# Kernel tuning notes

Measured on AMD Instinct MI355X. Metric: run time of the kernel, lower is better.

The kernel has to match this reference:

```python
import jax, jax.numpy as jnp
import numpy as np

K_V_DIM = 100
_SQRT_D = float(np.sqrt(K_V_DIM))


def _dk_layer(q, k, v, Wq, bq, Wk, n_unsqueeze):
    """One DKEncoder_layer: DK_text + DK_knowledge + DK_fusion (CokeBert attention).
    q: [B, q_dim]; k: [..., n, K_V_DIM]; v: [..., n, d_v].
    Attention over the last neighbor axis n.
    """
    # DK_text: linear + tanh + unsqueeze to broadcast against k
    q_i = jnp.tanh(q @ Wq.T + bq)                               # [B, D]
    q_i = q_i.reshape((q_i.shape[0],) + (1,) * n_unsqueeze + (K_V_DIM,))
    # DK_knowledge: bias-free linear on k
    k = k @ Wk.T
    # DK_fusion (CokeBert): scaled dot, mask zeros, leaky_relu+softmax, zero out fully-masked rows
    attn = (q_i * k).sum(-1) / _SQRT_D                          # [..., n]
    attn = jnp.where(attn == 0.0, -10000.0, attn)
    attn = jax.nn.softmax(jax.nn.leaky_relu(attn), axis=-1)
    n = attn.shape[-1]
    attn = jnp.where(attn == 1.0 / n, 0.0, attn)
    return jnp.einsum('...n,...nd->...d', attn, v)              # [..., d_v]


def setup_inputs() -> dict:
    key = jax.random.key(0)
    ks = jax.random.split(key, 12)
    B, S, E, N1, N2, D, Q = 8, 256, 256, 16, 16, K_V_DIM, 768
    return {
        "input_ent": jax.random.randint(ks[0], (B, S), 0, 2, dtype=jnp.int64),
        "q": jax.random.normal(ks[1], (B, S, Q), dtype=jnp.float32),
        "k1": jax.random.normal(ks[2], (B, E, N1, D), dtype=jnp.float32),
        "v1": jax.random.normal(ks[3], (B, E, N1, D), dtype=jnp.float32),
        "k2": jax.random.normal(ks[4], (B, E, N1, N2, D), dtype=jnp.float32),
        "v2": jax.random.normal(ks[5], (B, E, N1, N2, D), dtype=jnp.float32),
        # layers[0] has layer_no=2 (deepest), layers[1] has layer_no=1
        "Wq2": jax.random.normal(ks[6], (D, Q), dtype=jnp.float32) * 0.05,
        "bq2": jnp.zeros((D,), dtype=jnp.float32),
        "Wk2": jax.random.normal(ks[7], (D, D), dtype=jnp.float32) * 0.1,
        "Wq1": jax.random.normal(ks[8], (D, Q), dtype=jnp.float32) * 0.05,
        "bq1": jnp.zeros((D,), dtype=jnp.float32),
        "Wk1": jax.random.normal(ks[9], (D, D), dtype=jnp.float32) * 0.1,
    }


def reference(input_ent, q, k1, v1, k2, v2, Wq2, bq2, Wk2, Wq1, bq1, Wk1):
    q0 = q[:, 0, :]                                             # [B, Q]
    # layer 0 (layer_no=2): reduce innermost neighbor axis
    combined = _dk_layer(q0, k2, v2, Wq2, bq2, Wk2, 3)          # [B, E, N1, D]
    # layer 1 (layer_no=1): v = cat([v1, combined])
    v1c = jnp.concatenate([v1, combined], axis=-1)              # [B, E, N1, 2D]
    combined = _dk_layer(q0, k1, v1c, Wq1, bq1, Wk1, 2)         # [B, E, 2D]
    # scatter: i-th nonzero position of input_ent[b] receives combined[b, i]
    mask = input_ent != 0                                       # [B, S]
    rank = jnp.cumsum(mask.astype(jnp.int32), axis=1) - 1       # [B, S]
    rank = jnp.clip(rank, 0, combined.shape[1] - 1)
    gathered = jnp.take_along_axis(combined, rank[..., None], axis=1)  # [B, S, 2D]
    return jnp.where(mask[..., None], gathered, 0.0)
```

## Files before the change

### kernel.cpp

```cpp
#include <hip/hip_runtime.h>
#include <cstddef>
#include <cstdint>

#define BB 8
#define SS 256
#define EE 256
#define NN1 16
#define NN2 16
#define DD 100
#define QQ 768

__device__ __forceinline__ float dot4(float4 a, float4 b) {
    return a.x * b.x + a.y * b.y + a.z * b.z + a.w * b.w;
}

__global__ __launch_bounds__(256) void prep_kernel(
    const float* __restrict__ q, const int* __restrict__ ent,
    const float* __restrict__ Wq2, const float* __restrict__ bq2, const float* __restrict__ Wk2,
    const float* __restrict__ Wq1, const float* __restrict__ bq1, const float* __restrict__ Wk1,
    float* __restrict__ qk2o, float* __restrict__ qk1o, int* __restrict__ rk)
{
    const int blk = blockIdx.x, t = threadIdx.x;
    if (blk < 16) {
        const int b = blk >> 1, layer = blk & 1;
        const float* Wq = layer ? Wq1 : Wq2;
        const float* bq = layer ? bq1 : bq2;
        const float* Wk = layer ? Wk1 : Wk2;
        float* qko      = layer ? qk1o : qk2o;
        __shared__ float s_q[QQ];
        __shared__ float s_qi[DD];
        for (int i = t; i < QQ; i += 256) s_q[i] = q[(size_t)b * SS * QQ + i];
        __syncthreads();
        const float4* sq4 = (const float4*)s_q;
        const int r = t & 7;
        for (int d = t >> 3; d < DD; d += 32) {
            const float4* wq4 = (const float4*)(Wq + (size_t)d * QQ);
            float acc = 0.f;
            for (int c = r; c < QQ / 4; c += 8) acc += dot4(wq4[c], sq4[c]);
            acc += __shfl_xor(acc, 1, 8);
            acc += __shfl_xor(acc, 2, 8);
            acc += __shfl_xor(acc, 4, 8);
            if (r == 0) s_qi[d] = tanhf(acc + bq[d]);
        }
        __syncthreads();
        if (t < DD) {
            float acc = 0.f;
            for (int d = 0; d < DD; ++d) acc += s_qi[d] * Wk[d * DD + t];
            qko[b * DD + t] = 0.1f * acc;
        }
    } else {
        const int b = blk - 16;
        __shared__ int s_m[SS];
        const int m = (ent[b * SS + t] != 0) ? 1 : 0;
        s_m[t] = m;
        __syncthreads();
        for (int off = 1; off < SS; off <<= 1) {
            const int add = (t >= off) ? s_m[t - off] : 0;
            __syncthreads();
            s_m[t] += add;
            __syncthreads();
        }
        int rank = s_m[t] - 1;
        rank = rank < 0 ? 0 : (rank > EE - 1 ? EE - 1 : rank);
        rk[b * SS + t] = m ? rank : -1;
    }
}

__global__ __launch_bounds__(256) void dk2_kernel(
    const float* __restrict__ k2, const float* __restrict__ v2,
    const float* __restrict__ qk2g, float* __restrict__ c2o, int b0)
{
    const int blk = blockIdx.x;
    const int pi  = blk & 7;
    const int bbe = blk >> 3;
    const int b   = b0 + (bbe >> 8);
    const int be  = (b << 8) | (bbe & 255);
    const int t   = threadIdx.x;

    __shared__ float s_part[800];
    __shared__ float s_v[3200];
    __shared__ float s_logit[32];
    float4* sv4 = (float4*)s_v;

    const size_t tb = ((size_t)(be * NN1 + pi * 2)) * 400;
    const float4* kt  = (const float4*)k2 + tb;
    const float4* vt  = (const float4*)v2 + tb;
    const float4* qkb = (const float4*)qk2g + b * 25;

    const int i0 = t, i1 = t + 256, i2 = t + 512, i3 = t + 768;
    float4 ka0 = kt[i0], ka1 = kt[i1], ka2 = kt[i2];
    float4 va0 = vt[i0], va1 = vt[i1], va2 = vt[i2];
    float4 ka3, va3;
    if (t < 32) { ka3 = kt[i3]; va3 = vt[i3]; }
    const int c0 = i0 % 25, c1 = i1 % 25, c2 = i2 % 25, c3 = i3 % 25;
    const float4 q0 = qkb[c0], q1 = qkb[c1], q2 = qkb[c2], q3 = qkb[c3];

    s_part[i0] = dot4(ka0, q0); sv4[i0] = va0;
    s_part[i1] = dot4(ka1, q1); sv4[i1] = va1;
    s_part[i2] = dot4(ka2, q2); sv4[i2] = va2;
    if (t < 32) { s_part[i3] = dot4(ka3, q3); sv4[i3] = va3; }
    __syncthreads();

    if (t < 32) {
        float acc = 0.f;
        #pragma unroll
        for (int c = 0; c < 25; ++c) acc += s_part[t * 25 + c];
        if (acc == 0.0f) acc = -10000.0f;
        s_logit[t] = acc >= 0.f ? acc : 0.01f * acc;
    }
    __syncthreads();

    const int half = t >> 7;
    float lg = s_logit[half * 16 + (t & 15)];
    float mx = lg;
    mx = fmaxf(mx, __shfl_xor(mx, 1, 16));
    mx = fmaxf(mx, __shfl_xor(mx, 2, 16));
    mx = fmaxf(mx, __shfl_xor(mx, 4, 16));
    mx = fmaxf(mx, __shfl_xor(mx, 8, 16));
    const float e = __expf(lg - mx);
    float sm = e;
    sm += __shfl_xor(sm, 1, 16);
    sm += __shfl_xor(sm, 2, 16);
    sm += __shfl_xor(sm, 4, 16);
    sm += __shfl_xor(sm, 8, 16);
    float p = e / sm;
    if (p == 0.0625f) p = 0.f;
    float pn[16];
    #pragma unroll
    for (int n = 0; n < 16; ++n) pn[n] = __shfl(p, n, 16);

    const int lt = t & 127;
    if (lt < DD) {
        const float* vb = s_v + half * 1600;
        float a = 0.f;
        #pragma unroll
        for (int n = 0; n < NN2; ++n) a += pn[n] * vb[n * DD + lt];
        c2o[((size_t)bbe * NN1 + pi * 2 + half) * DD + lt] = a;
    }
}

__global__ __launch_bounds__(256) void dk1_kernel(
    const float* __restrict__ k1, const float* __restrict__ v1,
    const float* __restrict__ c2i, const float* __restrict__ qk1g,
    float* __restrict__ comb, int b0)
{
    const int bbe = blockIdx.x;
    const int b   = b0 + (bbe >> 8);
    const int be  = (b << 8) | (bbe & 255);
    const int t   = threadIdx.x;

    __shared__ float s_part[400];
    __shared__ float s_v[1600];
    __shared__ float s_c[1600];
    __shared__ float s_logit[16];
    float4* sv4 = (float4*)s_v;
    float4* sc4 = (float4*)s_c;

    const float4* kt  = (const float4*)k1 + (size_t)be * 400;
    const float4* vt  = (const float4*)v1 + (size_t)be * 400;
    const float4* ct  = (const float4*)c2i + (size_t)bbe * 400;
    const float4* qkb = (const float4*)qk1g + b * 25;

    const int i0 = t, i1 = t + 256;
    float4 ka0 = kt[i0], va0 = vt[i0], ca0 = ct[i0];
    float4 ka1, va1, ca1;
    if (t < 144) { ka1 = kt[i1]; va1 = vt[i1]; ca1 = ct[i1]; }
    const int c0 = i0 % 25, c1 = i1 % 25;
    const float4 q0 = qkb[c0], q1 = qkb[c1];

    s_part[i0] = dot4(ka0, q0); sv4[i0] = va0; sc4[i0] = ca0;
    if (t < 144) { s_part[i1] = dot4(ka1, q1); sv4[i1] = va1; sc4[i1] = ca1; }
    __syncthreads();

    if (t < 16) {
        float acc = 0.f;
        #pragma unroll
        for (int c = 0; c < 25; ++c) acc += s_part[t * 25 + c];
        if (acc == 0.0f) acc = -10000.0f;
        s_logit[t] = acc >= 0.f ? acc : 0.01f * acc;
    }
    __syncthreads();

    float lg = s_logit[t & 15];
    float mx = lg;
    mx = fmaxf(mx, __shfl_xor(mx, 1, 16));
    mx = fmaxf(mx, __shfl_xor(mx, 2, 16));
    mx = fmaxf(mx, __shfl_xor(mx, 4, 16));
    mx = fmaxf(mx, __shfl_xor(mx, 8, 16));
    const float e = __expf(lg - mx);
    float sm = e;
    sm += __shfl_xor(sm, 1, 16);
    sm += __shfl_xor(sm, 2, 16);
    sm += __shfl_xor(sm, 4, 16);
    sm += __shfl_xor(sm, 8, 16);
    float p = e / sm;
    if (p == 0.0625f) p = 0.f;
    float pn[16];
    #pragma unroll
    for (int n = 0; n < 16; ++n) pn[n] = __shfl(p, n, 16);

    if (t < 2 * DD) {
        float a = 0.f;
        if (t < DD) {
            #pragma unroll
            for (int n = 0; n < NN1; ++n) a += pn[n] * s_v[n * DD + t];
        } else {
            const int d = t - DD;
            #pragma unroll
            for (int n = 0; n < NN1; ++n) a += pn[n] * s_c[n * DD + d];
        }
        comb[(size_t)be * (2 * DD) + t] = a;
    }
}

__global__ __launch_bounds__(64) void gather_kernel(
    const float* __restrict__ comb, const int* __restrict__ rk, float* __restrict__ out)
{
    const int bs = blockIdx.x;
    const int b  = bs >> 8;
    const int t  = threadIdx.x;
    const int r  = rk[bs];
    float* o = out + (size_t)bs * (2 * DD);
    if (r < 0) {
        for (int d = t; d < 2 * DD; d += 64) o[d] = 0.f;
    } else {
        const float* src = comb + (size_t)(b * EE + r) * (2 * DD);
        for (int d = t; d < 2 * DD; d += 64) o[d] = src[d];
    }
}

extern "C" void kernel_launch(void* const* d_in, const int* in_sizes, int n_in,
                              void* d_out, int out_size, void* d_ws, size_t ws_size,
                              hipStream_t stream)
{
    const int*   ent = (const int*)d_in[0];
    const float* q   = (const float*)d_in[1];
    const float* k1  = (const float*)d_in[2];
    const float* v1  = (const float*)d_in[3];
    const float* k2  = (const float*)d_in[4];
    const float* v2  = (const float*)d_in[5];
    const float* Wq2 = (const float*)d_in[6];
    const float* bq2 = (const float*)d_in[7];
    const float* Wk2 = (const float*)d_in[8];
    const float* Wq1 = (const float*)d_in[9];
    const float* bq1 = (const float*)d_in[10];
    const float* Wk1 = (const float*)d_in[11];
    float* out = (float*)d_out;

    float* ws   = (float*)d_ws;
    float* qk2  = ws;
    float* qk1  = ws + 1024;
    int*   rk   = (int*)(ws + 2048);
    float* comb = ws + 4096;
    float* c2   = ws + 4096 + 409600;

    const size_t fixed = 4096 + 409600;
    const size_t perb  = (size_t)EE * NN1 * DD;
    size_t wsf = ws_size / sizeof(float);
    int kb = (wsf > fixed) ? (int)((wsf - fixed) / perb) : 1;
    if (kb < 1) kb = 1;
    if (kb > BB) kb = BB;

    prep_kernel<<<24, 256, 0, stream>>>(q, ent, Wq2, bq2, Wk2, Wq1, bq1, Wk1, qk2, qk1, rk);
    for (int b0 = 0; b0 < BB; b0 += kb) {
        const int nb = (BB - b0 < kb) ? (BB - b0) : kb;
        dk2_kernel<<<nb * EE * 8, 256, 0, stream>>>(k2, v2, qk2, c2, b0);
        dk1_kernel<<<nb * EE,     256, 0, stream>>>(k1, v1, c2, qk1, comb, b0);
    }
    gather_kernel<<<BB * SS, 64, 0, stream>>>(comb, rk, out);
}
```

Before: 146.5 us.

## Make dk2 kernel persistent with software-prefetched k tiles and cached q in LDS

Converts dk2 into a grid-stride persistent kernel with at most 2048 blocks. Each iteration prefetches the next unit's k tile into registers while the current unit's softmax and V reduction run. The qk2 vectors for all batches in the chunk are cached in shared memory, and the weighted V sum is restructured: V is scaled by p into LDS and reduced as float4 by 50 threads. Occupancy is pinned via launch bounds. The main risks are extra synchronisation and more LDS traffic per unit, and the s_q buffer relies on nb*DD fitting in 800 floats (nb up to 8).

```diff
diff --git a/kernel.cpp b/kernel.cpp
--- a/kernel.cpp
+++ b/kernel.cpp
@@ -66,76 +66,110 @@
     }
 }
 
-__global__ __launch_bounds__(256) void dk2_kernel(
+__global__ __launch_bounds__(256, 8) void dk2_kernel(
     const float* __restrict__ k2, const float* __restrict__ v2,
-    const float* __restrict__ qk2g, float* __restrict__ c2o, int b0)
-{
-    const int blk = blockIdx.x;
-    const int pi  = blk & 7;
-    const int bbe = blk >> 3;
-    const int b   = b0 + (bbe >> 8);
-    const int be  = (b << 8) | (bbe & 255);
-    const int t   = threadIdx.x;
-
-    __shared__ float s_part[800];
-    __shared__ float s_v[3200];
-    __shared__ float s_logit[32];
-    float4* sv4 = (float4*)s_v;
-
-    const size_t tb = ((size_t)(be * NN1 + pi * 2)) * 400;
-    const float4* kt  = (const float4*)k2 + tb;
-    const float4* vt  = (const float4*)v2 + tb;
-    const float4* qkb = (const float4*)qk2g + b * 25;
+    const float* __restrict__ qk2g, float* __restrict__ c2o,
+    int b0, int nb, int nunits)
+{
+    const int t = threadIdx.x;
+    __shared__ float  s_part[800];
+    __shared__ float4 s_pp[800];
+    __shared__ float  s_q[800];
+    __shared__ float  s_logit[32];
+    __shared__ float  s_p[32];
+
+    for (int i = t; i < nb * DD; i += 256) s_q[i] = qk2g[b0 * DD + i];
+    const float4* sq4 = (const float4*)s_q;
 
     const int i0 = t, i1 = t + 256, i2 = t + 512, i3 = t + 768;
-    float4 ka0 = kt[i0], ka1 = kt[i1], ka2 = kt[i2];
-    float4 va0 = vt[i0], va1 = vt[i1], va2 = vt[i2];
-    float4 ka3, va3;
-    if (t < 32) { ka3 = kt[i3]; va3 = vt[i3]; }
-    const int c0 = i0 % 25, c1 = i1 % 25, c2 = i2 % 25, c3 = i3 % 25;
-    const float4 q0 = qkb[c0], q1 = qkb[c1], q2 = qkb[c2], q3 = qkb[c3];
-
-    s_part[i0] = dot4(ka0, q0); sv4[i0] = va0;
-    s_part[i1] = dot4(ka1, q1); sv4[i1] = va1;
-    s_part[i2] = dot4(ka2, q2); sv4[i2] = va2;
-    if (t < 32) { s_part[i3] = dot4(ka3, q3); sv4[i3] = va3; }
+    const int c0 = i0 % 25, c1 = i1 % 25, c2x = i2 % 25, c3 = i3 % 25;
+    const int n0 = i0 / 25, n1_ = i1 / 25, n2_ = i2 / 25, n3_ = i3 / 25;
+
+    int u = blockIdx.x;
+    float4 ka0, ka1, ka2, ka3;
+    if (u < nunits) {
+        const int pi  = u & 7;
+        const int bbe = u >> 3;
+        const int be  = ((b0 + (bbe >> 8)) << 8) | (bbe & 255);
+        const float4* kt = (const float4*)k2 + ((size_t)(be * NN1 + pi * 2)) * 400;
+        ka0 = kt[i0]; ka1 = kt[i1]; ka2 = kt[i2];
+        if (t < 32) ka3 = kt[i3];
+    }
     __syncthreads();
 
-    if (t < 32) {
-        float acc = 0.f;
-        #pragma unroll
-        for (int c = 0; c < 25; ++c) acc += s_part[t * 25 + c];
-        if (acc == 0.0f) acc = -10000.0f;
-        s_logit[t] = acc >= 0.f ? acc : 0.01f * acc;
-    }
-    __syncthreads();
-
-    const int half = t >> 7;
-    float lg = s_logit[half * 16 + (t & 15)];
-    float mx = lg;
-    mx = fmaxf(mx, __shfl_xor(mx, 1, 16));
-    mx = fmaxf(mx, __shfl_xor(mx, 2, 16));
-    mx = fmaxf(mx, __shfl_xor(mx, 4, 16));
-    mx = fmaxf(mx, __shfl_xor(mx, 8, 16));
-    const float e = __expf(lg - mx);
-    float sm = e;
-    sm += __shfl_xor(sm, 1, 16);
-    sm += __shfl_xor(sm, 2, 16);
-    sm += __shfl_xor(sm, 4, 16);
-    sm += __shfl_xor(sm, 8, 16);
-    float p = e / sm;
-    if (p == 0.0625f) p = 0.f;
-    float pn[16];
-    #pragma unroll
-    for (int n = 0; n < 16; ++n) pn[n] = __shfl(p, n, 16);
-
-    const int lt = t & 127;
-    if (lt < DD) {
-        const float* vb = s_v + half * 1600;
-        float a = 0.f;
-        #pragma unroll
-        for (int n = 0; n < NN2; ++n) a += pn[n] * vb[n * DD + lt];
-        c2o[((size_t)bbe * NN1 + pi * 2 + half) * DD + lt] = a;
+    while (u < nunits) {
+        const int pi   = u & 7;
+        const int bbe  = u >> 3;
+        const int brel = bbe >> 8;
+        const int be   = ((b0 + brel) << 8) | (bbe & 255);
+        const size_t tb = ((size_t)(be * NN1 + pi * 2)) * 400;
+
+        const int qb = brel * 25;
+        s_part[i0] = dot4(ka0, sq4[qb + c0]);
+        s_part[i1] = dot4(ka1, sq4[qb + c1]);
+        s_part[i2] = dot4(ka2, sq4[qb + c2x]);
+        if (t < 32) s_part[i3] = dot4(ka3, sq4[qb + c3]);
+
+        const float4* vt = (const float4*)v2 + tb;
+        float4 va0 = vt[i0], va1 = vt[i1], va2 = vt[i2], va3;
+        if (t < 32) va3 = vt[i3];
+
+        const int un = u + gridDim.x;
+        if (un < nunits) {
+            const int pin  = un & 7;
+            const int bben = un >> 3;
+            const int ben  = ((b0 + (bben >> 8)) << 8) | (bben & 255);
+            const float4* ktn = (const float4*)k2 + ((size_t)(ben * NN1 + pin * 2)) * 400;
+            ka0 = ktn[i0]; ka1 = ktn[i1]; ka2 = ktn[i2];
+            if (t < 32) ka3 = ktn[i3];
+        }
+
+        __syncthreads();
+        if (t < 32) {
+            float acc = 0.f;
+            #pragma unroll
+            for (int c = 0; c < 25; ++c) acc += s_part[t * 25 + c];
+            if (acc == 0.0f) acc = -10000.0f;
+            s_logit[t] = acc >= 0.f ? acc : 0.01f * acc;
+        }
+        __syncthreads();
+        if (t < 32) {
+            const float lg = s_logit[t];
+            float mx = lg;
+            mx = fmaxf(mx, __shfl_xor(mx, 1, 16));
+            mx = fmaxf(mx, __shfl_xor(mx, 2, 16));
+            mx = fmaxf(mx, __shfl_xor(mx, 4, 16));
+            mx = fmaxf(mx, __shfl_xor(mx, 8, 16));
+            const float e = __expf(lg - mx);
+            float sm = e;
+            sm += __shfl_xor(sm, 1, 16);
+            sm += __shfl_xor(sm, 2, 16);
+            sm += __shfl_xor(sm, 4, 16);
+            sm += __shfl_xor(sm, 8, 16);
+            float p = e / sm;
+            if (p == 0.0625f) p = 0.f;
+            s_p[t] = p;
+        }
+        __syncthreads();
+        {
+            float p;
+            p = s_p[n0]; s_pp[i0] = make_float4(p*va0.x, p*va0.y, p*va0.z, p*va0.w);
+            p = s_p[n1_]; s_pp[i1] = make_float4(p*va1.x, p*va1.y, p*va1.z, p*va1.w);
+            p = s_p[n2_]; s_pp[i2] = make_float4(p*va2.x, p*va2.y, p*va2.z, p*va2.w);
+            if (t < 32) { p = s_p[n3_]; s_pp[i3] = make_float4(p*va3.x, p*va3.y, p*va3.z, p*va3.w); }
+        }
+        __syncthreads();
+        if (t < 50) {
+            const int h = t / 25, c = t % 25;
+            float4 a = make_float4(0.f, 0.f, 0.f, 0.f);
+            #pragma unroll
+            for (int n = 0; n < 16; ++n) {
+                const float4 x = s_pp[h * 400 + n * 25 + c];
+                a.x += x.x; a.y += x.y; a.z += x.z; a.w += x.w;
+            }
+            ((float4*)c2o)[((size_t)bbe * NN1 + pi * 2 + h) * 25 + c] = a;
+        }
+        u = un;
     }
 }
 
@@ -264,8 +298,10 @@
     prep_kernel<<<24, 256, 0, stream>>>(q, ent, Wq2, bq2, Wk2, Wq1, bq1, Wk1, qk2, qk1, rk);
     for (int b0 = 0; b0 < BB; b0 += kb) {
         const int nb = (BB - b0 < kb) ? (BB - b0) : kb;
-        dk2_kernel<<<nb * EE * 8, 256, 0, stream>>>(k2, v2, qk2, c2, b0);
-        dk1_kernel<<<nb * EE,     256, 0, stream>>>(k1, v1, c2, qk1, comb, b0);
+        const int nunits = nb * EE * 8;
+        const int grid = nunits < 2048 ? nunits : 2048;
+        dk2_kernel<<<grid, 256, 0, stream>>>(k2, v2, qk2, c2, b0, nb, nunits);
+        dk1_kernel<<<nb * EE, 256, 0, stream>>>(k1, v1, c2, qk1, comb, b0);
     }
     gather_kernel<<<BB * SS, 64, 0, stream>>>(comb, rk, out);
 }
```

After: 171.7 us. 17.2% more time.
